# Optimization experiments

Hardware: AMD Instinct MI355X
Metric: run time of the kernel (lower is better)

## Reference

```python
import jax, jax.numpy as jnp
import numpy as np
import math

B, S, DM, H = 4, 4096, 1024, 16
HD = DM // H  # 64

def setup_inputs() -> dict:
    key = jax.random.key(0)
    ks = jax.random.split(key, 5)
    def xavier(k, shape):
        bound = math.sqrt(6.0 / (shape[0] + shape[1]))
        return jax.random.uniform(k, shape, jnp.float32, -bound, bound)
    return {
        "x": jax.random.normal(ks[0], (B, S, DM), jnp.float32),
        "Wq": xavier(ks[1], (DM, DM)),
        "Wk": xavier(ks[2], (DM, DM)),
        "Wv": xavier(ks[3], (DM, DM)),
        "Wfc": xavier(ks[4], (DM, DM)),
    }

def reference(x, Wq, Wk, Wv, Wfc):
    b, s, dm = x.shape
    h, hd = H, dm // H
    # nn.Linear(no bias): x @ W.T, then view [B, S, H, HD]
    Q = (x @ Wq.T).reshape(b, s, h, hd)
    K = (x @ Wk.T).reshape(b, s, h, hd)
    V = (x @ Wv.T).reshape(b, s, h, hd)
    # NOTE: faithful to original — no head transpose, so attention is over heads axis.
    # scores: [B, S, H, H]
    scores = jnp.einsum('bshd,bstd->bsht', Q, K) / math.sqrt(hd)
    attn = jax.nn.softmax(scores, axis=-1)
    # dropout is identity in eval mode
    out = jnp.einsum('bsht,bstd->bshd', attn, V).reshape(b, s, dm)
    return out @ Wfc.T
```

## Files before the change

### kernel.cpp

```cpp
#include <hip/hip_runtime.h>

typedef unsigned short u16;
typedef unsigned int u32;
typedef short bf16x8 __attribute__((ext_vector_type(8)));
typedef float f32x4 __attribute__((ext_vector_type(4)));

#define BN 128

__device__ __forceinline__ u16 f2bf(float f) {
    u32 u = __float_as_uint(f);
    u32 r = (u + 0x7fffu + ((u >> 16) & 1u)) >> 16;
    return (u16)r;
}

__device__ __forceinline__ void gld_lds16(const void* g, void* s) {
    __builtin_amdgcn_global_load_lds(
        (__attribute__((address_space(1))) void*)(g),
        (__attribute__((address_space(3))) void*)(s),
        16, 0, 0);
}

__global__ void cast_all(const float* __restrict__ x,
                         const float* __restrict__ wq, const float* __restrict__ wk,
                         const float* __restrict__ wv, const float* __restrict__ wfc,
                         u16* __restrict__ xb, u16* __restrict__ wqkvb, u16* __restrict__ wfcb) {
    size_t g = (size_t)blockIdx.x * 256 + threadIdx.x;
    const float* s;
    u16* d;
    size_t off;
    if (g < 4194304u) {
        s = x; d = xb; off = g;
    } else {
        size_t w = g - 4194304u;
        int y = (int)(w >> 18);
        off = w & 262143u;
        s = (y == 0) ? wq : (y == 1) ? wk : (y == 2) ? wv : wfc;
        d = (y < 3) ? (wqkvb + (size_t)y * 1048576u) : wfcb;
    }
    float4 v = ((const float4*)s)[off];
    ushort4 o;
    o.x = f2bf(v.x); o.y = f2bf(v.y); o.z = f2bf(v.z); o.w = f2bf(v.w);
    *(ushort4*)(d + off * 4) = o;
}

template <int BMT, int MODE>
__global__ __launch_bounds__(256, 2)
void gemm_bt(const u16* __restrict__ A, const u16* __restrict__ B,
             void* __restrict__ C0, void* __restrict__ C1, int M, int N, int K) {
    constexpr int WMT = BMT / 32;
    __shared__ __align__(16) u16 As[BMT * 64];
    __shared__ __align__(16) u16 Bs[BN * 64];

    const int tid  = threadIdx.x;
    const int lane = tid & 63;
    const int wave = tid >> 6;
    const int wm = wave >> 1, wn = wave & 1;
    const int bm = blockIdx.y * BMT;
    const int bn = blockIdx.x * BN;

    const int srow   = lane >> 3;
    const int schunk = (lane & 7) ^ srow;

    f32x4 acc[WMT][4];
#pragma unroll
    for (int i = 0; i < WMT; ++i)
#pragma unroll
        for (int j = 0; j < 4; ++j) acc[i][j] = (f32x4){0.f, 0.f, 0.f, 0.f};

    const int nkt = K >> 6;
    for (int kt = 0; kt < nkt; ++kt) {
        const int k0 = kt << 6;
        __syncthreads();
#pragma unroll
        for (int j = 0; j < WMT; ++j) {
            const int r = j * 32 + wave * 8;
            gld_lds16(A + (size_t)(bm + r + srow) * K + k0 + schunk * 8, &As[r * 64]);
        }
#pragma unroll
        for (int j = 0; j < 4; ++j) {
            const int r = j * 32 + wave * 8;
            gld_lds16(B + (size_t)(bn + r + srow) * K + k0 + schunk * 8, &Bs[r * 64]);
        }
        __syncthreads();
#pragma unroll
        for (int kk = 0; kk < 2; ++kk) {
            const int c = kk * 4 + (lane >> 4);
            bf16x8 af[WMT], bfr[4];
#pragma unroll
            for (int i = 0; i < WMT; ++i) {
                int m = wm * (WMT * 16) + i * 16 + (lane & 15);
                af[i] = *(const bf16x8*)&As[m * 64 + ((c ^ (m & 7)) << 3)];
            }
#pragma unroll
            for (int j = 0; j < 4; ++j) {
                int n = wn * 64 + j * 16 + (lane & 15);
                bfr[j] = *(const bf16x8*)&Bs[n * 64 + ((c ^ (n & 7)) << 3)];
            }
#pragma unroll
            for (int i = 0; i < WMT; ++i)
#pragma unroll
                for (int j = 0; j < 4; ++j)
                    acc[i][j] = __builtin_amdgcn_mfma_f32_16x16x32_bf16(
                        af[i], bfr[j], acc[i][j], 0, 0, 0);
        }
    }

    const int cr = (lane >> 4) * 4;
    const int cc = lane & 15;
#pragma unroll
    for (int i = 0; i < WMT; ++i) {
#pragma unroll
        for (int j = 0; j < 4; ++j) {
            const int row0 = bm + wm * (WMT * 16) + i * 16 + cr;
            const int col  = bn + wn * 64 + j * 16 + cc;
#pragma unroll
            for (int r = 0; r < 4; ++r) {
                float v = acc[i][j][r];
                const int row = row0 + r;
                if (MODE == 0) {
                    if (col < 2048)
                        ((u16*)C0)[(size_t)row * 2048 + col] = f2bf(v);
                    else
                        ((u16*)C1)[(size_t)row * 1024 + (col - 2048)] = f2bf(v);
                } else {
                    ((float*)C0)[(size_t)row * N + col] = v;
                }
            }
        }
    }
}

__global__ __launch_bounds__(256)
void attn_kernel(const u16* __restrict__ QK, const u16* __restrict__ V,
                 u16* __restrict__ O) {
    __shared__ __align__(16) u16 sQ[4][16 * 80];
    __shared__ __align__(16) u16 sK[4][16 * 80];
    __shared__ __align__(16) u16 sV[4][64 * 16];
    __shared__ __align__(16) u16 sP[4][16 * 16];

    const int lane = threadIdx.x & 63;
    const int wave = threadIdx.x >> 6;
    const size_t m = (size_t)blockIdx.x * 4 + wave;
    const u16* bqk = QK + m * 2048;
    const u16* bv  = V + m * 1024;

#pragma unroll
    for (int c6 = 0; c6 < 4; ++c6) {
        int chunk = c6 * 64 + lane;
        uint4 v = *(const uint4*)(bqk + chunk * 8);
        int cc = chunk & 127;
        int row = cc >> 3, pch = cc & 7;
        u16* dst = (chunk < 128) ? sQ[wave] : sK[wave];
        *(uint4*)&dst[row * 80 + pch * 8] = v;
    }
#pragma unroll
    for (int c6 = 0; c6 < 2; ++c6) {
        int cc = c6 * 64 + lane;
        int t = cc >> 3, d0 = (cc & 7) * 8;
        uint4 v = *(const uint4*)(bv + cc * 8);
        u16 e[8]; *(uint4*)e = v;
#pragma unroll
        for (int k = 0; k < 8; ++k) {
            int d = d0 + k;
            int blk = (t >> 3) ^ ((d >> 3) & 1);
            sV[wave][d * 16 + blk * 8 + (t & 7)] = e[k];
        }
    }
    __syncthreads();

    const int ln = lane & 15;
    const int g  = lane >> 4;

    f32x4 s = (f32x4){0.f, 0.f, 0.f, 0.f};
    {
        bf16x8 a0 = *(const bf16x8*)&sK[wave][ln * 80 + g * 8];
        bf16x8 b0 = *(const bf16x8*)&sQ[wave][ln * 80 + g * 8];
        s = __builtin_amdgcn_mfma_f32_16x16x32_bf16(a0, b0, s, 0, 0, 0);
        bf16x8 a1 = *(const bf16x8*)&sK[wave][ln * 80 + 32 + g * 8];
        bf16x8 b1 = *(const bf16x8*)&sQ[wave][ln * 80 + 32 + g * 8];
        s = __builtin_amdgcn_mfma_f32_16x16x32_bf16(a1, b1, s, 0, 0, 0);
    }
    float sv[4];
#pragma unroll
    for (int r = 0; r < 4; ++r) sv[r] = s[r] * 0.125f;

    float mx = fmaxf(fmaxf(sv[0], sv[1]), fmaxf(sv[2], sv[3]));
    mx = fmaxf(mx, __shfl_xor(mx, 16));
    mx = fmaxf(mx, __shfl_xor(mx, 32));
    float e[4], sum = 0.f;
#pragma unroll
    for (int r = 0; r < 4; ++r) { e[r] = __expf(sv[r] - mx); sum += e[r]; }
    sum += __shfl_xor(sum, 16);
    sum += __shfl_xor(sum, 32);
    const float inv = 1.f / sum;

    ushort4 pb;
    pb.x = f2bf(e[0] * inv); pb.y = f2bf(e[1] * inv);
    pb.z = f2bf(e[2] * inv); pb.w = f2bf(e[3] * inv);
    *(ushort4*)&sP[wave][ln * 16 + g * 4] = pb;
    __syncthreads();

    bf16x8 bl = *(const bf16x8*)&sP[wave][ln * 16 + (g & 1) * 8];
    bf16x8 bz = (bf16x8){0, 0, 0, 0, 0, 0, 0, 0};
    bf16x8 bp = (g < 2) ? bl : bz;

#pragma unroll
    for (int dt = 0; dt < 4; ++dt) {
        int d = dt * 16 + ln;
        int blk = (g & 1) ^ ((d >> 3) & 1);
        bf16x8 av = *(const bf16x8*)&sV[wave][d * 16 + blk * 8];
        f32x4 o = __builtin_amdgcn_mfma_f32_16x16x32_bf16(
            av, bp, (f32x4){0.f, 0.f, 0.f, 0.f}, 0, 0, 0);
        ushort4 ob;
        ob.x = f2bf(o[0]); ob.y = f2bf(o[1]);
        ob.z = f2bf(o[2]); ob.w = f2bf(o[3]);
        *(ushort4*)(O + m * 1024 + ln * 64 + dt * 16 + g * 4) = ob;
    }
}

extern "C" void kernel_launch(void* const* d_in, const int* in_sizes, int n_in,
                              void* d_out, int out_size, void* d_ws, size_t ws_size,
                              hipStream_t stream) {
    const float* x   = (const float*)d_in[0];
    const float* Wq  = (const float*)d_in[1];
    const float* Wk  = (const float*)d_in[2];
    const float* Wv  = (const float*)d_in[3];
    const float* Wfc = (const float*)d_in[4];

    const int M = 16384, K = 1024, NQKV = 3072, N2 = 1024;

    char* ws = (char*)d_ws;
    u16* xb    = (u16*)ws;
    u16* wqkvb = (u16*)(ws + 33554432);
    u16* wfcb  = (u16*)(ws + 33554432 + 6291456);
    u16* vbuf  = (u16*)(ws + 33554432 + 6291456 + 2097152);
    u16* qkbuf = (u16*)d_out;

    cast_all<<<20480, 256, 0, stream>>>(x, Wq, Wk, Wv, Wfc, xb, wqkvb, wfcb);

    gemm_bt<128, 0><<<dim3(NQKV / BN, M / 128), 256, 0, stream>>>(
        xb, wqkvb, qkbuf, vbuf, M, NQKV, K);

    u16* Ob = xb;
    attn_kernel<<<M / 4, 256, 0, stream>>>(qkbuf, vbuf, Ob);

    gemm_bt<256, 1><<<dim3(N2 / BN, M / 256), 256, 0, stream>>>(
        Ob, wfcb, d_out, nullptr, M, N2, K);
}
```

Before: 294.2 us.

## Rewrite bf16 GEMM as 256x256 tile, 8-wave, 4-stage pipelined kernel

After: 296.5 us. About the same (+0.8%).

```diff
diff --git a/kernel.cpp b/kernel.cpp
--- a/kernel.cpp
+++ b/kernel.cpp
@@ -4,8 +4,6 @@
 typedef unsigned int u32;
 typedef short bf16x8 __attribute__((ext_vector_type(8)));
 typedef float f32x4 __attribute__((ext_vector_type(4)));
-
-#define BN 128
 
 __device__ __forceinline__ u16 f2bf(float f) {
     u32 u = __float_as_uint(f);
@@ -43,75 +41,114 @@
     *(ushort4*)(d + off * 4) = o;
 }
 
-template <int BMT, int MODE>
-__global__ __launch_bounds__(256, 2)
-void gemm_bt(const u16* __restrict__ A, const u16* __restrict__ B,
-             void* __restrict__ C0, void* __restrict__ C1, int M, int N, int K) {
-    constexpr int WMT = BMT / 32;
-    __shared__ __align__(16) u16 As[BMT * 64];
-    __shared__ __align__(16) u16 Bs[BN * 64];
+template <int MODE>
+__global__ __launch_bounds__(512, 2)
+void gemm_bt8(const u16* __restrict__ A, const u16* __restrict__ B,
+              void* __restrict__ C0, void* __restrict__ C1,
+              int M, int N, int K) {
+    __shared__ __align__(16) u16 sA[4][8192];
+    __shared__ __align__(16) u16 sB[4][8192];
 
     const int tid  = threadIdx.x;
     const int lane = tid & 63;
     const int wave = tid >> 6;
-    const int wm = wave >> 1, wn = wave & 1;
-    const int bm = blockIdx.y * BMT;
-    const int bn = blockIdx.x * BN;
-
-    const int srow   = lane >> 3;
-    const int schunk = (lane & 7) ^ srow;
-
-    f32x4 acc[WMT][4];
-#pragma unroll
-    for (int i = 0; i < WMT; ++i)
+    const int wm = wave >> 2;
+    const int wn = wave & 3;
+
+    const int ntx = N >> 8;
+    const int cpx = gridDim.x >> 3;
+    const int swz = ((int)blockIdx.x & 7) * cpx + ((int)blockIdx.x >> 3);
+    const int bm = (swz / ntx) << 8;
+    const int bn = (swz % ntx) << 8;
+
+    const int srow = tid >> 2;
+    const int sch  = (tid & 3) ^ ((srow >> 1) & 3);
+    const u16* a0 = A + (size_t)(bm +       srow) * K + sch * 8;
+    const u16* a1 = A + (size_t)(bm + 128 + srow) * K + sch * 8;
+    const u16* b0 = B + (size_t)(bn +       srow) * K + sch * 8;
+    const u16* b1 = B + (size_t)(bn + 128 + srow) * K + sch * 8;
+    const int ldst = tid * 8;
+
+    auto stA = [&](int t) {
+        u16* d = &sA[t & 3][0];
+        gld_lds16(a0 + t * 32, d + ldst);
+        gld_lds16(a1 + t * 32, d + 4096 + ldst);
+    };
+    auto stB = [&](int t) {
+        u16* d = &sB[t & 3][0];
+        gld_lds16(b0 + t * 32, d + ldst);
+        gld_lds16(b1 + t * 32, d + 4096 + ldst);
+    };
+
+    const int l15 = lane & 15;
+    const int sc8 = (((lane >> 4) ^ ((l15 >> 1) & 3)) << 3);
+    const int arow = wm * 128 + l15;
+    const int brow = wn * 64  + l15;
+
+    f32x4 acc[8][4];
+#pragma unroll
+    for (int i = 0; i < 8; ++i)
 #pragma unroll
         for (int j = 0; j < 4; ++j) acc[i][j] = (f32x4){0.f, 0.f, 0.f, 0.f};
 
-    const int nkt = K >> 6;
-    for (int kt = 0; kt < nkt; ++kt) {
-        const int k0 = kt << 6;
-        __syncthreads();
-#pragma unroll
-        for (int j = 0; j < WMT; ++j) {
-            const int r = j * 32 + wave * 8;
-            gld_lds16(A + (size_t)(bm + r + srow) * K + k0 + schunk * 8, &As[r * 64]);
-        }
+    const int T = K >> 5;
+
+    stA(0); stB(0); stA(1); stB(1); stA(2); stB(2);
+    asm volatile("s_waitcnt vmcnt(8)" ::: "memory");
+    asm volatile("s_barrier" ::: "memory");
+
+    for (int w = 0; w < T; ++w) {
+        const u16* pa = &sA[w & 3][0];
+        const u16* pb = &sB[w & 3][0];
+
+        bf16x8 af[4], bf[4];
+#pragma unroll
+        for (int i = 0; i < 4; ++i)
+            af[i] = *(const bf16x8*)&pa[(arow + i * 16) * 32 + sc8];
+#pragma unroll
+        for (int j = 0; j < 4; ++j)
+            bf[j] = *(const bf16x8*)&pb[(brow + j * 16) * 32 + sc8];
+        if (w + 3 < T) stA(w + 3);
+        asm volatile("s_barrier" ::: "memory");
+        asm volatile("s_waitcnt lgkmcnt(0)" ::: "memory");
+        __builtin_amdgcn_s_setprio(1);
+#pragma unroll
+        for (int i = 0; i < 4; ++i)
+#pragma unroll
+            for (int j = 0; j < 4; ++j)
+                acc[i][j] = __builtin_amdgcn_mfma_f32_16x16x32_bf16(
+                    af[i], bf[j], acc[i][j], 0, 0, 0);
+        __builtin_amdgcn_s_setprio(0);
+        asm volatile("s_barrier" ::: "memory");
+
+        bf16x8 ag[4];
+#pragma unroll
+        for (int i = 0; i < 4; ++i)
+            ag[i] = *(const bf16x8*)&pa[(arow + (i + 4) * 16) * 32 + sc8];
+        if (w + 3 < T) stB(w + 3);
+        if (w < T - 3)       asm volatile("s_waitcnt vmcnt(8)" ::: "memory");
+        else if (w == T - 3) asm volatile("s_waitcnt vmcnt(4)" ::: "memory");
+        else if (w == T - 2) asm volatile("s_waitcnt vmcnt(0)" ::: "memory");
+        asm volatile("s_barrier" ::: "memory");
+        asm volatile("s_waitcnt lgkmcnt(0)" ::: "memory");
+        __builtin_amdgcn_s_setprio(1);
+#pragma unroll
+        for (int i = 0; i < 4; ++i)
+#pragma unroll
+            for (int j = 0; j < 4; ++j)
+                acc[i + 4][j] = __builtin_amdgcn_mfma_f32_16x16x32_bf16(
+                    ag[i], bf[j], acc[i + 4][j], 0, 0, 0);
+        __builtin_amdgcn_s_setprio(0);
+        asm volatile("s_barrier" ::: "memory");
+    }
+
+    const int cr = (lane >> 4) * 4;
+    const int cc = l15;
+#pragma unroll
+    for (int i = 0; i < 8; ++i) {
 #pragma unroll
         for (int j = 0; j < 4; ++j) {
-            const int r = j * 32 + wave * 8;
-            gld_lds16(B + (size_t)(bn + r + srow) * K + k0 + schunk * 8, &Bs[r * 64]);
-        }
-        __syncthreads();
-#pragma unroll
-        for (int kk = 0; kk < 2; ++kk) {
-            const int c = kk * 4 + (lane >> 4);
-            bf16x8 af[WMT], bfr[4];
-#pragma unroll
-            for (int i = 0; i < WMT; ++i) {
-                int m = wm * (WMT * 16) + i * 16 + (lane & 15);
-                af[i] = *(const bf16x8*)&As[m * 64 + ((c ^ (m & 7)) << 3)];
-            }
-#pragma unroll
-            for (int j = 0; j < 4; ++j) {
-                int n = wn * 64 + j * 16 + (lane & 15);
-                bfr[j] = *(const bf16x8*)&Bs[n * 64 + ((c ^ (n & 7)) << 3)];
-            }
-#pragma unroll
-            for (int i = 0; i < WMT; ++i)
-#pragma unroll
-                for (int j = 0; j < 4; ++j)
-                    acc[i][j] = __builtin_amdgcn_mfma_f32_16x16x32_bf16(
-                        af[i], bfr[j], acc[i][j], 0, 0, 0);
-        }
-    }
-
-    const int cr = (lane >> 4) * 4;
-    const int cc = lane & 15;
-#pragma unroll
-    for (int i = 0; i < WMT; ++i) {
-#pragma unroll
-        for (int j = 0; j < 4; ++j) {
-            const int row0 = bm + wm * (WMT * 16) + i * 16 + cr;
+            const int row0 = bm + wm * 128 + i * 16 + cr;
             const int col  = bn + wn * 64 + j * 16 + cc;
 #pragma unroll
             for (int r = 0; r < 4; ++r) {
@@ -238,12 +275,10 @@
 
     cast_all<<<20480, 256, 0, stream>>>(x, Wq, Wk, Wv, Wfc, xb, wqkvb, wfcb);
 
-    gemm_bt<128, 0><<<dim3(NQKV / BN, M / 128), 256, 0, stream>>>(
-        xb, wqkvb, qkbuf, vbuf, M, NQKV, K);
+    gemm_bt8<0><<<768, 512, 0, stream>>>(xb, wqkvb, qkbuf, vbuf, M, NQKV, K);
 
     u16* Ob = xb;
     attn_kernel<<<M / 4, 256, 0, stream>>>(qkbuf, vbuf, Ob);
 
-    gemm_bt<256, 1><<<dim3(N2 / BN, M / 256), 256, 0, stream>>>(
-        Ob, wfcb, d_out, nullptr, M, N2, K);
-}
+    gemm_bt8<1><<<256, 512, 0, stream>>>(Ob, wfcb, d_out, nullptr, M, N2, K);
+}
```
